# Optimization experiments

Hardware: AMD Instinct MI355X
Metric: run time of the kernel (lower is better)

## Reference

```python
import jax, jax.numpy as jnp
import numpy as np

DIM = 768
HEADS = 12
HD = DIM // HEADS
B = 8
N = 1025  # 1 cls token + 32x32 patch grid
NUM_CLS = 1
ROPE_BASE = 100.0


def setup_inputs() -> dict:
    key = jax.random.key(0)
    ks = jax.random.split(key, 4)
    x = jax.random.normal(ks[0], (B, N, DIM), jnp.float32)
    xpos = jax.random.randint(ks[1], (B, N, 2), 0, 32)  # int 2D grid coords
    mask_for_attention = jnp.ones((B, N, N), dtype=bool)
    w_qkv = jax.random.normal(ks[2], (3 * DIM, DIM), jnp.float32) / np.sqrt(DIM)
    w_proj = jax.random.normal(ks[3], (DIM, DIM), jnp.float32) / np.sqrt(DIM)
    b_proj = jnp.zeros((DIM,), jnp.float32)
    return {"num_cls": NUM_CLS, "x": x, "xpos": xpos,
            "mask_for_attention": mask_for_attention,
            "w_qkv": w_qkv, "w_proj": w_proj, "b_proj": b_proj}


def _rope1d(t, pos):
    # t: [B,H,N,d], pos: [B,N] float. croco-style: cos/sin table of size d = cat(f,f),
    # rotate_half(x) = cat(-x2, x1).
    d = t.shape[-1]
    inv = 1.0 / (ROPE_BASE ** (jnp.arange(0, d, 2, dtype=jnp.float32) / d))  # [d/2]
    ang = pos[..., None] * inv  # [B,N,d/2]
    cos = jnp.concatenate([jnp.cos(ang), jnp.cos(ang)], -1)[:, None]  # [B,1,N,d]
    sin = jnp.concatenate([jnp.sin(ang), jnp.sin(ang)], -1)[:, None]
    t1, t2 = jnp.split(t, 2, -1)
    rot = jnp.concatenate([-t2, t1], -1)
    return t * cos + rot * sin


def _rope2d(t, pos):
    # first half of head_dim rotated by y coord, second half by x coord
    d = t.shape[-1] // 2
    py = pos[..., 0].astype(t.dtype)
    px = pos[..., 1].astype(t.dtype)
    return jnp.concatenate([_rope1d(t[..., :d], py), _rope1d(t[..., d:], px)], -1)


def reference(num_cls, x, xpos, mask_for_attention, w_qkv, w_proj, b_proj):
    Bb, Nn, C = x.shape
    H, hd = HEADS, C // HEADS
    scale = hd ** -0.5
    # qkv projection -> [B,H,3,N,hd] (mirrors torch .transpose(1,3))
    qkv = (x @ w_qkv.T).reshape(Bb, Nn, 3, H, hd).transpose(0, 3, 2, 1, 4)
    q, k, v = qkv[:, :, 0], qkv[:, :, 1], qkv[:, :, 2]
    # RoPE on non-cls tokens only
    q_nc = _rope2d(q[:, :, num_cls:], xpos[:, num_cls:])
    k_nc = _rope2d(k[:, :, num_cls:], xpos[:, num_cls:])
    # block-structured sim matrix
    sim_rope = jnp.einsum('bhqd,bhkd->bhqk', q_nc, k_nc)            # [B,H,N-c,N-c]
    sim_qcls_k = jnp.einsum('bhqd,bhkd->bhqk', q[:, :, :num_cls], k[:, :, num_cls:])  # [B,H,c,N-c]
    sim_q = jnp.einsum('bhqd,bhkd->bhqk', q, k[:, :, :num_cls])      # [B,H,N,c]
    sim = jnp.concatenate([sim_q,
                           jnp.concatenate([sim_qcls_k, sim_rope], axis=-2)],
                          axis=-1)  # [B,H,N,N]
    sim = sim * scale
    sim = jnp.where(mask_for_attention[:, None], sim, -jnp.inf)
    attn = jax.nn.softmax(sim, axis=-1)
    out = jnp.einsum('bhqk,bhkd->bhqd', attn, v)
    out = out.transpose(0, 2, 1, 3).reshape(Bb, Nn, C)
    return out @ w_proj.T + b_proj
```

## Files before the change

kernel.cpp:

```cpp
#include <hip/hip_runtime.h>

#define Bb 8
#define Nn 1025
#define Hh 12
#define HD 64
#define DIMC 768
#define QKVC 2304
#define MROWS (Bb * Nn)
#define MPADA 8320
#define VNP 1024
#define K1 0.180336880111f
#define RBLK ((Bb * Hh * Nn + 3) / 4)
#define VTBLK ((VNP / 64) * Bb * Hh)

typedef _Float16 f16x8 __attribute__((ext_vector_type(8)));
typedef _Float16 f16x4 __attribute__((ext_vector_type(4)));
typedef float f32x4 __attribute__((ext_vector_type(4)));

typedef const __attribute__((address_space(1))) void gv_t;
typedef __attribute__((address_space(3))) void lv_t;

static __device__ __forceinline__ float fast_exp2(float x) {
    return __builtin_amdgcn_exp2f(x);
}

__global__ void cvt3_kernel(const float* __restrict__ s0, _Float16* __restrict__ d0, int n0,
                            const float* __restrict__ s1, _Float16* __restrict__ d1, int n1,
                            const float* __restrict__ s2, _Float16* __restrict__ d2, int n2) {
    int i = blockIdx.x * 256 + threadIdx.x;
    const float* s; _Float16* d; int j;
    if (i < n0)           { s = s0; d = d0; j = i; }
    else if (i < n0 + n1) { s = s1; d = d1; j = i - n0; }
    else if (i < n0 + n1 + n2) { s = s2; d = d2; j = i - n0 - n1; }
    else return;
    float4 v = ((const float4*)s)[j];
    f16x4 h;
    h.x = (_Float16)v.x; h.y = (_Float16)v.y; h.z = (_Float16)v.z; h.w = (_Float16)v.w;
    ((f16x4*)d)[j] = h;
}

template <int MODE>
__global__ void __launch_bounds__(256) gemm_kernel(
    const _Float16* __restrict__ A, const _Float16* __restrict__ W,
    int M, int Ncols, int K,
    _Float16* __restrict__ outh, const float* __restrict__ bias, float* __restrict__ outf)
{
    __shared__ _Float16 As[2][128 * 32];
    __shared__ _Float16 Ws[2][128 * 32];
    const int tid = threadIdx.x;
    const int wid = tid >> 6, lane = tid & 63;
    const int quad = lane >> 4, l16 = lane & 15;
    const int bm = blockIdx.x * 128, bn = blockIdx.y * 128;
    const int wm = (wid >> 1) * 64, wn = (wid & 1) * 64;

    f32x4 acc[4][4] = {};

    for (int kk = 0; kk < K; kk += 64) {
#pragma unroll
        for (int half = 0; half < 2; ++half) {
#pragma unroll
            for (int c = 0; c < 2; ++c) {
                int s = c * 256 + tid;
                int row = s >> 2, gr = s & 3;
                const _Float16* ga = A + (size_t)(bm + row) * K + kk + half * 32 + gr * 8;
                const _Float16* gw = W + (size_t)(bn + row) * K + kk + half * 32 + gr * 8;
                _Float16* la = As[half] + (size_t)(c * 256 + wid * 64) * 8;
                _Float16* lw = Ws[half] + (size_t)(c * 256 + wid * 64) * 8;
                __builtin_amdgcn_global_load_lds((gv_t*)ga, (lv_t*)la, 16, 0, 0);
                __builtin_amdgcn_global_load_lds((gv_t*)gw, (lv_t*)lw, 16, 0, 0);
            }
        }
        __syncthreads();

#pragma unroll
        for (int half = 0; half < 2; ++half) {
            f16x8 af[4], bf[4];
#pragma unroll
            for (int t = 0; t < 4; ++t) {
                af[t] = *(const f16x8*)(As[half] + (size_t)(wm + t * 16 + l16) * 32 + quad * 8);
                bf[t] = *(const f16x8*)(Ws[half] + (size_t)(wn + t * 16 + l16) * 32 + quad * 8);
            }
#pragma unroll
            for (int tm = 0; tm < 4; ++tm)
#pragma unroll
                for (int tn = 0; tn < 4; ++tn)
                    acc[tm][tn] = __builtin_amdgcn_mfma_f32_16x16x32_f16(af[tm], bf[tn], acc[tm][tn], 0, 0, 0);
        }
        __syncthreads();
    }

#pragma unroll
    for (int tm = 0; tm < 4; ++tm) {
#pragma unroll
        for (int r = 0; r < 4; ++r) {
            int row = bm + wm + tm * 16 + quad * 4 + r;
            if (row >= M) continue;
#pragma unroll
            for (int tn = 0; tn < 4; ++tn) {
                int col = bn + wn + tn * 16 + l16;
                float val = acc[tm][tn][r];
                if (MODE == 0) {
                    outh[(size_t)row * Ncols + col] = (_Float16)val;
                } else {
                    outf[(size_t)row * Ncols + col] = val + bias[col];
                }
            }
        }
    }
}

__global__ void __launch_bounds__(256) ropevtrans_kernel(
    _Float16* __restrict__ qkv, const int* __restrict__ xpos,
    float* __restrict__ col0, float* __restrict__ row0, _Float16* __restrict__ vt)
{
    __shared__ _Float16 Ts[64][72];
    const int blk = blockIdx.x;
    const int tid = threadIdx.x;

    if (blk < RBLK) {
        int gw = blk * 4 + (tid >> 6);
        int lane = tid & 63;
        if (gw >= Bb * Hh * Nn) return;
        int n = gw % Nn;
        int bh = gw / Nn;
        int b = bh / Hh, h = bh - b * Hh;

        _Float16* qp = qkv + ((size_t)b * Nn + n) * QKVC + h * HD;
        _Float16* kp = qp + DIMC;
        const _Float16* qp0 = qkv + (size_t)b * Nn * QKVC + h * HD;
        const _Float16* kp0 = qp0 + DIMC;

        float q = (float)qp[lane];
        float k = (float)kp[lane];
        float q0 = (float)qp0[lane];
        float k0 = (float)kp0[lane];

        float dcol = q * k0, drow = q0 * k;
#pragma unroll
        for (int off = 1; off < 64; off <<= 1) {
            dcol += __shfl_xor(dcol, off);
            drow += __shfl_xor(drow, off);
        }
        if (lane == 0) {
            col0[gw] = dcol * K1;
            row0[gw] = drow * K1;
        }

        if (n >= 1) {
            int py = xpos[((size_t)b * Nn + n) * 2 + 0];
            int px = xpos[((size_t)b * Nn + n) * 2 + 1];
            float pos = (lane < 32) ? (float)py : (float)px;
            int j = lane & 15;
            float inv = __expf(-0.28782313662f * (float)j);
            float ang = pos * inv;
            float sv = __sinf(ang), cv = __cosf(ang);
            float qp_ = __shfl_xor(q, 16);
            float kp_ = __shfl_xor(k, 16);
            float sgn = (lane & 16) ? 1.0f : -1.0f;
            qp[lane] = (_Float16)((q * cv + sgn * qp_ * sv) * K1);
            kp[lane] = (_Float16)(k * cv + sgn * kp_ * sv);
        }
    } else {
        int idx = blk - RBLK;
        int nt = idx % (VNP / 64);
        int bh = idx / (VNP / 64);
        int b = bh / Hh, h = bh - b * Hh;
        int n0 = nt * 64;
        const _Float16* vsrc = qkv + (size_t)b * Nn * QKVC + 2 * DIMC + h * HD;
#pragma unroll
        for (int i = 0; i < 2; ++i) {
            int t = tid + i * 256;
            int r = t >> 3, cg = t & 7;
            f16x8 v8 = *(const f16x8*)(vsrc + (size_t)(n0 + r) * QKVC + cg * 8);
            *(f16x8*)&Ts[r][cg * 8] = v8;
        }
        __syncthreads();
#pragma unroll
        for (int i = 0; i < 2; ++i) {
            int t = tid + i * 256;
            int d = t >> 3, ng = t & 7;
            f16x8 o;
#pragma unroll
            for (int s = 0; s < 8; ++s) o[s] = Ts[ng * 8 + s][d];
            *(f16x8*)(vt + ((size_t)bh * HD + d) * VNP + n0 + ng * 8) = o;
        }
    }
}

__global__ void __launch_bounds__(256) flash_kernel(
    const _Float16* __restrict__ qkv, const _Float16* __restrict__ vt,
    const float* __restrict__ col0, const float* __restrict__ row0,
    _Float16* __restrict__ att)
{
    __shared__ _Float16 Ks[128][72];
    __shared__ _Float16 Vt[64][136];
    __shared__ _Float16 Ps[64][136];

    const int qt = blockIdx.x, bh = blockIdx.y;
    const int b = bh / Hh, h = bh - b * Hh;
    const int tid = threadIdx.x, wid = tid >> 6, lane = tid & 63;
    const int quad = lane >> 4, l16 = lane & 15;
    const int q0row = qt * 64;
    const int c0base = bh * Nn;
    const _Float16* qg = qkv + (size_t)b * Nn * QKVC + h * HD;
    const _Float16* kg = qg + DIMC;
    const _Float16* vtg = vt + (size_t)bh * HD * VNP;

    const int kR = tid >> 3, kC = (tid & 7) * 8;
    const int vD = tid >> 4, vC = (tid & 15) * 8;

#pragma unroll
    for (int i = 0; i < 2; ++i) {
        int t = tid + i * 256;
        int r = t >> 3, cg = t & 7;
        int gr = q0row + r;
        f16x8 v8 = {};
        if (gr < Nn) v8 = *(const f16x8*)(qg + (size_t)gr * QKVC + cg * 8);
        *(f16x8*)&Ks[r][cg * 8] = v8;
    }
    __syncthreads();
    f16x8 aq[2];
#pragma unroll
    for (int ks = 0; ks < 2; ++ks)
        aq[ks] = *(const f16x8*)&Ks[wid * 16 + l16][ks * 32 + quad * 8];
    __syncthreads();

    f32x4 oacc[4] = {};
    float lrow[4] = {0.f, 0.f, 0.f, 0.f};
    const int gibase = q0row + wid * 16 + quad * 4;

    f16x8 kreg[4], vreg[4];
#pragma unroll
    for (int i = 0; i < 4; ++i) {
        kreg[i] = *(const f16x8*)(kg + (size_t)(kR + i * 32) * QKVC + kC);
        vreg[i] = *(const f16x8*)(vtg + (size_t)(vD + i * 16) * VNP + vC);
    }

    for (int c0 = 0; c0 < VNP; c0 += 128) {
#pragma unroll
        for (int i = 0; i < 4; ++i) {
            *(f16x8*)&Ks[kR + i * 32][kC] = kreg[i];
            *(f16x8*)&Vt[vD + i * 16][vC] = vreg[i];
        }
        __syncthreads();

        int cn = c0 + 128;
        if (cn < VNP) {
#pragma unroll
            for (int i = 0; i < 4; ++i) {
                kreg[i] = *(const f16x8*)(kg + (size_t)(cn + kR + i * 32) * QKVC + kC);
                vreg[i] = *(const f16x8*)(vtg + (size_t)(vD + i * 16) * VNP + cn + vC);
            }
        }

        f32x4 sacc[8] = {};
#pragma unroll
        for (int ks = 0; ks < 2; ++ks)
#pragma unroll
            for (int ct = 0; ct < 8; ++ct) {
                f16x8 bk = *(const f16x8*)&Ks[ct * 16 + l16][ks * 32 + quad * 8];
                sacc[ct] = __builtin_amdgcn_mfma_f32_16x16x32_f16(aq[ks], bk, sacc[ct], 0, 0, 0);
            }

        if (c0 == 0 && l16 == 0) {
#pragma unroll
            for (int r = 0; r < 4; ++r) {
                int gi = gibase + r;
                sacc[0][r] = col0[c0base + (gi < Nn ? gi : 0)];
            }
        }
        if (q0row == 0 && wid == 0 && quad == 0) {
#pragma unroll
            for (int ct = 0; ct < 8; ++ct)
                sacc[ct][0] = row0[c0base + c0 + ct * 16 + l16];
        }

#pragma unroll
        for (int ct = 0; ct < 8; ++ct) {
#pragma unroll
            for (int r = 0; r < 4; ++r) {
                float p = fast_exp2(sacc[ct][r]);
                lrow[r] += p;
                Ps[wid * 16 + quad * 4 + r][ct * 16 + l16] = (_Float16)p;
            }
        }

#pragma unroll
        for (int ks = 0; ks < 4; ++ks) {
            f16x8 ap = *(const f16x8*)&Ps[wid * 16 + l16][ks * 32 + quad * 8];
#pragma unroll
            for (int ct = 0; ct < 4; ++ct) {
                f16x8 bv = *(const f16x8*)&Vt[ct * 16 + l16][ks * 32 + quad * 8];
                oacc[ct] = __builtin_amdgcn_mfma_f32_16x16x32_f16(ap, bv, oacc[ct], 0, 0, 0);
            }
        }
        __syncthreads();
    }

    {
        const _Float16* k1 = kg + (size_t)1024 * QKVC;
        f16x8 kk0 = *(const f16x8*)(k1 + quad * 8);
        f16x8 kk1 = *(const f16x8*)(k1 + 32 + quad * 8);
        float part = 0.f;
#pragma unroll
        for (int j = 0; j < 8; ++j)
            part += (float)aq[0][j] * (float)kk0[j] + (float)aq[1][j] * (float)kk1[j];
        part += __shfl_xor(part, 16);
        part += __shfl_xor(part, 32);
        float s = part;
        if (q0row == 0 && wid == 0 && l16 == 0) s = row0[c0base + 1024];
        float p = fast_exp2(s);
#pragma unroll
        for (int r = 0; r < 4; ++r)
            if (quad == (l16 >> 2) && (l16 & 3) == r) lrow[r] += p;
        const _Float16* v1 = qg + 2 * DIMC + (size_t)1024 * QKVC;
        float vv[4];
#pragma unroll
        for (int ct = 0; ct < 4; ++ct) vv[ct] = (float)v1[ct * 16 + l16];
#pragma unroll
        for (int r = 0; r < 4; ++r) {
            float pr = __shfl(p, quad * 4 + r);
#pragma unroll
            for (int ct = 0; ct < 4; ++ct) oacc[ct][r] += pr * vv[ct];
        }
    }

#pragma unroll
    for (int r = 0; r < 4; ++r) {
        float l = lrow[r];
#pragma unroll
        for (int off = 1; off < 16; off <<= 1) l += __shfl_xor(l, off);
        int gi = q0row + wid * 16 + quad * 4 + r;
        if (gi >= Nn) continue;
        float inv_l = 1.0f / l;
#pragma unroll
        for (int ct = 0; ct < 4; ++ct) {
            att[((size_t)b * Nn + gi) * DIMC + h * HD + ct * 16 + l16] =
                (_Float16)(oacc[ct][r] * inv_l);
        }
    }
}

extern "C" void kernel_launch(void* const* d_in, const int* in_sizes, int n_in,
                              void* d_out, int out_size, void* d_ws, size_t ws_size,
                              hipStream_t stream) {
    const float* x      = (const float*)d_in[1];
    const int*   xpos   = (const int*)d_in[2];
    const float* w_qkv  = (const float*)d_in[4];
    const float* w_proj = (const float*)d_in[5];
    const float* b_proj = (const float*)d_in[6];
    float* out = (float*)d_out;

    char* ws = (char*)d_ws;
    size_t off = 0;
    auto alloc = [&](size_t bytes) {
        char* p = ws + off;
        off += (bytes + 255) & ~(size_t)255;
        return p;
    };
    _Float16* xh     = (_Float16*)alloc((size_t)MPADA * DIMC * 2);
    _Float16* qkvh   = (_Float16*)alloc((size_t)MROWS * QKVC * 2);
    _Float16* vt     = (_Float16*)alloc((size_t)Bb * Hh * HD * VNP * 2);
    _Float16* wqkvh  = (_Float16*)alloc((size_t)3 * DIMC * DIMC * 2);
    _Float16* wprojh = (_Float16*)alloc((size_t)DIMC * DIMC * 2);
    float* col0      = (float*)alloc((size_t)Bb * Hh * Nn * 4);
    float* row0      = (float*)alloc((size_t)Bb * Hh * Nn * 4);
    _Float16* atth   = xh;

    {
        int n0 = (MROWS * DIMC) / 4;
        int n1 = (3 * DIMC * DIMC) / 4;
        int n2 = (DIMC * DIMC) / 4;
        int nt = n0 + n1 + n2;
        cvt3_kernel<<<(nt + 255) / 256, 256, 0, stream>>>(
            x, xh, n0, w_qkv, wqkvh, n1, w_proj, wprojh, n2);
    }

    gemm_kernel<0><<<dim3(MPADA / 128, QKVC / 128), 256, 0, stream>>>(
        xh, wqkvh, MROWS, QKVC, DIMC, qkvh, nullptr, nullptr);

    ropevtrans_kernel<<<RBLK + VTBLK, 256, 0, stream>>>(
        qkvh, xpos, col0, row0, vt);

    flash_kernel<<<dim3((Nn + 63) / 64, Bb * Hh), 256, 0, stream>>>(
        qkvh, vt, col0, row0, atth);

    gemm_kernel<1><<<dim3(MPADA / 128, DIMC / 128), 256, 0, stream>>>(
        atth, wprojh, MROWS, DIMC, DIMC, nullptr, b_proj, out);
}
```

Before: 279.8 us.

## Process 128 query rows per flash-attention block to reuse K/V tiles

The flash-attention kernel now covers 128 query rows per block instead of 64. Each wave holds two 16-row query fragments and accumulators, and each 128-key tile is processed as two 64-column halves so the P buffer stays small. This halves K/V global loads and LDS staging per query row, and makes each loaded K/V fragment feed two MFMAs. In exchange it uses more registers per thread, launches fewer blocks, and wastes more work on the final 128-row tile, which holds only one real row.

```diff
diff --git a/kernel.cpp b/kernel.cpp
--- a/kernel.cpp
+++ b/kernel.cpp
@@ -194,13 +194,13 @@
 {
     __shared__ _Float16 Ks[128][72];
     __shared__ _Float16 Vt[64][136];
-    __shared__ _Float16 Ps[64][136];
+    __shared__ _Float16 Ps[128][72];
 
     const int qt = blockIdx.x, bh = blockIdx.y;
     const int b = bh / Hh, h = bh - b * Hh;
     const int tid = threadIdx.x, wid = tid >> 6, lane = tid & 63;
     const int quad = lane >> 4, l16 = lane & 15;
-    const int q0row = qt * 64;
+    const int q0row = qt * 128;
     const int c0base = bh * Nn;
     const _Float16* qg = qkv + (size_t)b * Nn * QKVC + h * HD;
     const _Float16* kg = qg + DIMC;
@@ -210,7 +210,7 @@
     const int vD = tid >> 4, vC = (tid & 15) * 8;
 
 #pragma unroll
-    for (int i = 0; i < 2; ++i) {
+    for (int i = 0; i < 4; ++i) {
         int t = tid + i * 256;
         int r = t >> 3, cg = t & 7;
         int gr = q0row + r;
@@ -219,15 +219,16 @@
         *(f16x8*)&Ks[r][cg * 8] = v8;
     }
     __syncthreads();
-    f16x8 aq[2];
-#pragma unroll
-    for (int ks = 0; ks < 2; ++ks)
-        aq[ks] = *(const f16x8*)&Ks[wid * 16 + l16][ks * 32 + quad * 8];
+    f16x8 aq[2][2];
+#pragma unroll
+    for (int q2 = 0; q2 < 2; ++q2)
+#pragma unroll
+        for (int ks = 0; ks < 2; ++ks)
+            aq[q2][ks] = *(const f16x8*)&Ks[q2 * 64 + wid * 16 + l16][ks * 32 + quad * 8];
     __syncthreads();
 
-    f32x4 oacc[4] = {};
-    float lrow[4] = {0.f, 0.f, 0.f, 0.f};
-    const int gibase = q0row + wid * 16 + quad * 4;
+    f32x4 oacc[2][4] = {};
+    float lrow[2][4] = {{0.f,0.f,0.f,0.f},{0.f,0.f,0.f,0.f}};
 
     f16x8 kreg[4], vreg[4];
 #pragma unroll
@@ -253,90 +254,103 @@
             }
         }
 
-        f32x4 sacc[8] = {};
-#pragma unroll
-        for (int ks = 0; ks < 2; ++ks)
-#pragma unroll
-            for (int ct = 0; ct < 8; ++ct) {
-                f16x8 bk = *(const f16x8*)&Ks[ct * 16 + l16][ks * 32 + quad * 8];
-                sacc[ct] = __builtin_amdgcn_mfma_f32_16x16x32_f16(aq[ks], bk, sacc[ct], 0, 0, 0);
-            }
-
-        if (c0 == 0 && l16 == 0) {
-#pragma unroll
-            for (int r = 0; r < 4; ++r) {
-                int gi = gibase + r;
-                sacc[0][r] = col0[c0base + (gi < Nn ? gi : 0)];
-            }
-        }
-        if (q0row == 0 && wid == 0 && quad == 0) {
-#pragma unroll
-            for (int ct = 0; ct < 8; ++ct)
-                sacc[ct][0] = row0[c0base + c0 + ct * 16 + l16];
-        }
-
-#pragma unroll
-        for (int ct = 0; ct < 8; ++ct) {
-#pragma unroll
-            for (int r = 0; r < 4; ++r) {
-                float p = fast_exp2(sacc[ct][r]);
-                lrow[r] += p;
-                Ps[wid * 16 + quad * 4 + r][ct * 16 + l16] = (_Float16)p;
-            }
-        }
-
-#pragma unroll
-        for (int ks = 0; ks < 4; ++ks) {
-            f16x8 ap = *(const f16x8*)&Ps[wid * 16 + l16][ks * 32 + quad * 8];
-#pragma unroll
-            for (int ct = 0; ct < 4; ++ct) {
-                f16x8 bv = *(const f16x8*)&Vt[ct * 16 + l16][ks * 32 + quad * 8];
-                oacc[ct] = __builtin_amdgcn_mfma_f32_16x16x32_f16(ap, bv, oacc[ct], 0, 0, 0);
+#pragma unroll
+        for (int sub = 0; sub < 2; ++sub) {
+            f32x4 sacc[2][4] = {};
+#pragma unroll
+            for (int ks = 0; ks < 2; ++ks)
+#pragma unroll
+                for (int ct = 0; ct < 4; ++ct) {
+                    f16x8 bk = *(const f16x8*)&Ks[sub * 64 + ct * 16 + l16][ks * 32 + quad * 8];
+                    sacc[0][ct] = __builtin_amdgcn_mfma_f32_16x16x32_f16(aq[0][ks], bk, sacc[0][ct], 0, 0, 0);
+                    sacc[1][ct] = __builtin_amdgcn_mfma_f32_16x16x32_f16(aq[1][ks], bk, sacc[1][ct], 0, 0, 0);
+                }
+
+            if (c0 == 0 && sub == 0 && l16 == 0) {
+#pragma unroll
+                for (int q2 = 0; q2 < 2; ++q2)
+#pragma unroll
+                    for (int r = 0; r < 4; ++r) {
+                        int gi = q0row + q2 * 64 + wid * 16 + quad * 4 + r;
+                        sacc[q2][0][r] = col0[c0base + (gi < Nn ? gi : 0)];
+                    }
+            }
+            if (q0row == 0 && wid == 0 && quad == 0) {
+#pragma unroll
+                for (int ct = 0; ct < 4; ++ct)
+                    sacc[0][ct][0] = row0[c0base + c0 + sub * 64 + ct * 16 + l16];
+            }
+
+#pragma unroll
+            for (int q2 = 0; q2 < 2; ++q2)
+#pragma unroll
+                for (int ct = 0; ct < 4; ++ct) {
+#pragma unroll
+                    for (int r = 0; r < 4; ++r) {
+                        float p = fast_exp2(sacc[q2][ct][r]);
+                        lrow[q2][r] += p;
+                        Ps[q2 * 64 + wid * 16 + quad * 4 + r][ct * 16 + l16] = (_Float16)p;
+                    }
+                }
+
+#pragma unroll
+            for (int ks = 0; ks < 2; ++ks) {
+                f16x8 ap0 = *(const f16x8*)&Ps[wid * 16 + l16][ks * 32 + quad * 8];
+                f16x8 ap1 = *(const f16x8*)&Ps[64 + wid * 16 + l16][ks * 32 + quad * 8];
+                int kglob = sub * 2 + ks;
+#pragma unroll
+                for (int ct = 0; ct < 4; ++ct) {
+                    f16x8 bv = *(const f16x8*)&Vt[ct * 16 + l16][kglob * 32 + quad * 8];
+                    oacc[0][ct] = __builtin_amdgcn_mfma_f32_16x16x32_f16(ap0, bv, oacc[0][ct], 0, 0, 0);
+                    oacc[1][ct] = __builtin_amdgcn_mfma_f32_16x16x32_f16(ap1, bv, oacc[1][ct], 0, 0, 0);
+                }
             }
         }
         __syncthreads();
     }
 
-    {
-        const _Float16* k1 = kg + (size_t)1024 * QKVC;
-        f16x8 kk0 = *(const f16x8*)(k1 + quad * 8);
-        f16x8 kk1 = *(const f16x8*)(k1 + 32 + quad * 8);
+    const _Float16* k1 = kg + (size_t)1024 * QKVC;
+    f16x8 kk0 = *(const f16x8*)(k1 + quad * 8);
+    f16x8 kk1 = *(const f16x8*)(k1 + 32 + quad * 8);
+    const _Float16* v1 = qg + 2 * DIMC + (size_t)1024 * QKVC;
+    float vv[4];
+#pragma unroll
+    for (int ct = 0; ct < 4; ++ct) vv[ct] = (float)v1[ct * 16 + l16];
+
+#pragma unroll
+    for (int q2 = 0; q2 < 2; ++q2) {
         float part = 0.f;
 #pragma unroll
         for (int j = 0; j < 8; ++j)
-            part += (float)aq[0][j] * (float)kk0[j] + (float)aq[1][j] * (float)kk1[j];
+            part += (float)aq[q2][0][j] * (float)kk0[j] + (float)aq[q2][1][j] * (float)kk1[j];
         part += __shfl_xor(part, 16);
         part += __shfl_xor(part, 32);
         float s = part;
-        if (q0row == 0 && wid == 0 && l16 == 0) s = row0[c0base + 1024];
+        if (q0row == 0 && q2 == 0 && wid == 0 && l16 == 0) s = row0[c0base + 1024];
         float p = fast_exp2(s);
 #pragma unroll
         for (int r = 0; r < 4; ++r)
-            if (quad == (l16 >> 2) && (l16 & 3) == r) lrow[r] += p;
-        const _Float16* v1 = qg + 2 * DIMC + (size_t)1024 * QKVC;
-        float vv[4];
-#pragma unroll
-        for (int ct = 0; ct < 4; ++ct) vv[ct] = (float)v1[ct * 16 + l16];
+            if (quad == (l16 >> 2) && (l16 & 3) == r) lrow[q2][r] += p;
 #pragma unroll
         for (int r = 0; r < 4; ++r) {
             float pr = __shfl(p, quad * 4 + r);
 #pragma unroll
-            for (int ct = 0; ct < 4; ++ct) oacc[ct][r] += pr * vv[ct];
-        }
-    }
-
-#pragma unroll
-    for (int r = 0; r < 4; ++r) {
-        float l = lrow[r];
-#pragma unroll
-        for (int off = 1; off < 16; off <<= 1) l += __shfl_xor(l, off);
-        int gi = q0row + wid * 16 + quad * 4 + r;
-        if (gi >= Nn) continue;
-        float inv_l = 1.0f / l;
-#pragma unroll
-        for (int ct = 0; ct < 4; ++ct) {
-            att[((size_t)b * Nn + gi) * DIMC + h * HD + ct * 16 + l16] =
-                (_Float16)(oacc[ct][r] * inv_l);
+            for (int ct = 0; ct < 4; ++ct) oacc[q2][ct][r] += pr * vv[ct];
+        }
+
+#pragma unroll
+        for (int r = 0; r < 4; ++r) {
+            float l = lrow[q2][r];
+#pragma unroll
+            for (int off = 1; off < 16; off <<= 1) l += __shfl_xor(l, off);
+            int gi = q0row + q2 * 64 + wid * 16 + quad * 4 + r;
+            if (gi >= Nn) continue;
+            float inv_l = 1.0f / l;
+#pragma unroll
+            for (int ct = 0; ct < 4; ++ct) {
+                att[((size_t)b * Nn + gi) * DIMC + h * HD + ct * 16 + l16] =
+                    (_Float16)(oacc[q2][ct][r] * inv_l);
+            }
         }
     }
 }
@@ -382,7 +396,7 @@
     ropevtrans_kernel<<<RBLK + VTBLK, 256, 0, stream>>>(
         qkvh, xpos, col0, row0, vt);
 
-    flash_kernel<<<dim3((Nn + 63) / 64, Bb * Hh), 256, 0, stream>>>(
+    flash_kernel<<<dim3((Nn + 127) / 128, Bb * Hh), 256, 0, stream>>>(
         qkvh, vt, col0, row0, atth);
 
     gemm_kernel<1><<<dim3(MPADA / 128, DIMC / 128), 256, 0, stream>>>(
```

Result: no change. 283.3 us (+1.2%).
